# Performance work log

Hardware: AMD Instinct MI355X
Metric: run time of the kernel (lower is better)

The kernel has to match this reference:

```python
import jax, jax.numpy as jnp
import numpy as np


def setup_inputs() -> dict:
    key = jax.random.key(0)
    k1, k2, k3 = jax.random.split(key, 3)
    B, H, S, D = 2, 16, 2048, 64
    q = jax.random.normal(k1, (B, H, S, D), dtype=jnp.float32)
    k = jax.random.normal(k2, (B, H, S, D), dtype=jnp.float32)
    v = jax.random.normal(k3, (B, H, S, D), dtype=jnp.float32)
    return {"q": q, "k": k, "v": v}


def reference(q, k, v):
    # q,k,v: [B,H,S,D]; causal attention with 1/sqrt(D) scaling, fp32 softmax.
    scale = 1.0 / (q.shape[-1] ** 0.5)
    scores = jnp.einsum('bhqd,bhkd->bhqk', q * scale, k)  # [B,H,S,S]
    S = scores.shape[-1]
    causal_mask = jnp.triu(jnp.ones((S, S), dtype=bool), k=1)
    scores = jnp.where(causal_mask, -jnp.inf, scores)
    attn = jax.nn.softmax(scores.astype(jnp.float32), axis=-1).astype(q.dtype)
    output = jnp.einsum('bhqk,bhkd->bhqd', attn, v)
    # Module also returns an all-zeros attn_weights placeholder of shape [B,H,S,S]
    attn_weights = jnp.zeros(scores.shape, dtype=q.dtype)
    return (output, attn_weights)
```

## Files before the change

kernel.cpp:

```cpp
#include <hip/hip_runtime.h>


typedef __bf16 bf16x8 __attribute__((ext_vector_type(8)));
typedef float f32x4 __attribute__((ext_vector_type(4)));

#define LOG2E 1.44269504088896340736f

__device__ __forceinline__ unsigned short f2bf(float f) {
  unsigned int u = __float_as_uint(f);
  u += 0x7fffu + ((u >> 16) & 1u);
  return (unsigned short)(u >> 16);
}

__device__ __forceinline__ void block_sync_lds() {
  asm volatile("s_waitcnt lgkmcnt(0)" ::: "memory");
  __builtin_amdgcn_s_barrier();
}

__device__ __forceinline__ float redmax_q(float x) {
  float a = x, b = x;
  asm volatile("" : "+v"(b));
  asm("v_permlane16_swap_b32 %0, %1" : "+v"(a), "+v"(b));
  float m = fmaxf(a, b);
  float c = m, d = m;
  asm volatile("" : "+v"(d));
  asm("v_permlane32_swap_b32 %0, %1" : "+v"(c), "+v"(d));
  return fmaxf(c, d);
}
__device__ __forceinline__ float redsum_q(float x) {
  float a = x, b = x;
  asm volatile("" : "+v"(b));
  asm("v_permlane16_swap_b32 %0, %1" : "+v"(a), "+v"(b));
  float s = a + b;
  float c = s, d = s;
  asm volatile("" : "+v"(d));
  asm("v_permlane32_swap_b32 %0, %1" : "+v"(c), "+v"(d));
  return c + d;
}

constexpr int Sdim = 2048, Ddim = 64, BHn = 32;
constexpr int STiles = 16;
constexpr int LDA = 68;
constexpr int OUT0 = BHn * Sdim * Ddim;
constexpr int NCOMPUTE = BHn * STiles;
constexpr int NFILL = 1024;
constexpr size_t FILL_F4_PER_BLK = 32768;

__device__ __forceinline__ int vswz_m(int d) { return ((d >> 2) ^ (d >> 5)) & 7; }
__device__ __forceinline__ int vrow(int d) { return (d & 56) | ((d ^ (d >> 3)) & 7); }

__global__ __launch_bounds__(256, 3)
void flash_causal_kernel(const float* __restrict__ Q, const float* __restrict__ K,
                         const float* __restrict__ V, float* __restrict__ out) {
  __shared__ unsigned short Klds[2][64 * LDA];
  __shared__ unsigned short Vlds[2][64 * LDA];
  __shared__ unsigned short Plds[4][2][16 * LDA];

  const int tid = threadIdx.x;
  const int b   = (int)blockIdx.x;

  if (b >= NCOMPUTE) {
    const int fidx = b - NCOMPUTE;
    f32x4* zp = (f32x4*)(out + OUT0) + (size_t)fidx * FILL_F4_PER_BLK;
    const f32x4 z4 = (f32x4){0.f, 0.f, 0.f, 0.f};
    #pragma unroll 4
    for (size_t i = tid; i < FILL_F4_PER_BLK; i += 256)
      __builtin_nontemporal_store(z4, zp + i);
    return;
  }

  const int wave = tid >> 6;
  const int lane = tid & 63;
  const int quad = lane >> 4;
  const int l15  = lane & 15;

  const int bh = b & (BHn - 1);
  const int g  = b >> 5;
  const int s  = (g & 1) ? (STiles - 1) - (g >> 1) : (g >> 1);
  const int jmax = 2 * s + 1;

  const int base  = bh * Sdim * Ddim;
  const int qbase = s * 128;

  bf16x8 aq[2][2];
  #pragma unroll
  for (int f = 0; f < 2; ++f) {
    const float* qp = Q + base + (qbase + 64 * f + wave * 16 + l15) * Ddim + quad * 8;
    #pragma unroll
    for (int s2 = 0; s2 < 2; ++s2) {
      float4 a = *(const float4*)(qp + 32 * s2);
      float4 bq = *(const float4*)(qp + 32 * s2 + 4);
      union { unsigned short u[8]; bf16x8 v; } u;
      u.u[0] = f2bf(a.x * 0.125f);  u.u[1] = f2bf(a.y * 0.125f);
      u.u[2] = f2bf(a.z * 0.125f);  u.u[3] = f2bf(a.w * 0.125f);
      u.u[4] = f2bf(bq.x * 0.125f); u.u[5] = f2bf(bq.y * 0.125f);
      u.u[6] = f2bf(bq.z * 0.125f); u.u[7] = f2bf(bq.w * 0.125f);
      aq[f][s2] = u.v;
    }
  }

  f32x4 ot[2][4];
  #pragma unroll
  for (int f = 0; f < 2; ++f)
    #pragma unroll
    for (int t = 0; t < 4; ++t) ot[f][t] = (f32x4){0.f, 0.f, 0.f, 0.f};
  float mrun[2] = {-__builtin_inff(), -__builtin_inff()};
  float lrun[2] = {0.f, 0.f};

  const float4* kg4 = (const float4*)(K + base);
  const float4* vg4 = (const float4*)(V + base);
  float4 kf[4], vf[4];

  auto ldtile = [&](int j) {
    const float4* kp = kg4 + j * 1024;
    const float4* vp = vg4 + j * 1024;
    #pragma unroll
    for (int i = 0; i < 4; ++i) { kf[i] = kp[i * 256 + tid]; vf[i] = vp[i * 256 + tid]; }
  };
  auto stage = [&](int buf) {
    #pragma unroll
    for (int i = 0; i < 4; ++i) {
      int lin = i * 256 + tid;
      int row = lin >> 4;
      int c4  = (lin & 15) << 2;
      uint2 t2;
      t2.x = (unsigned int)f2bf(kf[i].x) | ((unsigned int)f2bf(kf[i].y) << 16);
      t2.y = (unsigned int)f2bf(kf[i].z) | ((unsigned int)f2bf(kf[i].w) << 16);
      *(uint2*)&Klds[buf][row * LDA + c4] = t2;
      const int sw = vswz_m(c4) << 3;
      Vlds[buf][vrow(c4 + 0) * LDA + (row ^ sw)] = f2bf(vf[i].x);
      Vlds[buf][vrow(c4 + 1) * LDA + (row ^ sw)] = f2bf(vf[i].y);
      Vlds[buf][vrow(c4 + 2) * LDA + (row ^ sw)] = f2bf(vf[i].z);
      Vlds[buf][vrow(c4 + 3) * LDA + (row ^ sw)] = f2bf(vf[i].w);
    }
  };

  ldtile(0); stage(0); ldtile(1);

  for (int j = 0; j <= jmax; ++j) {
    block_sync_lds();
    if (j < jmax) stage((j + 1) & 1);
    if (j + 2 <= jmax) ldtile(j + 2);

    const unsigned short* Kb = Klds[j & 1];
    const unsigned short* Vb = Vlds[j & 1];
    const bool f0act = (j <= 2 * s);

    f32x4 sc[2][4];
    #pragma unroll
    for (int f = 0; f < 2; ++f)
      #pragma unroll
      for (int t = 0; t < 4; ++t) sc[f][t] = (f32x4){0.f, 0.f, 0.f, 0.f};
    __builtin_amdgcn_s_setprio(1);
    #pragma unroll
    for (int s2 = 0; s2 < 2; ++s2) {
      #pragma unroll
      for (int t = 0; t < 4; ++t) {
        bf16x8 ka = *(const bf16x8*)&Kb[(16 * t + l15) * LDA + 32 * s2 + quad * 8];
        sc[0][t] = __builtin_amdgcn_mfma_f32_16x16x32_bf16(ka, aq[0][s2], sc[0][t], 0, 0, 0);
        sc[1][t] = __builtin_amdgcn_mfma_f32_16x16x32_bf16(ka, aq[1][s2], sc[1][t], 0, 0, 0);
      }
    }
    __builtin_amdgcn_s_setprio(0);

    #pragma unroll
    for (int f = 0; f < 2; ++f) {
      if (j == 2 * s + f) {
        const int qml = wave * 16 + l15;
        #pragma unroll
        for (int t = 0; t < 4; ++t)
          #pragma unroll
          for (int r = 0; r < 4; ++r)
            if (16 * t + 4 * quad + r > qml) sc[f][t][r] = -__builtin_inff();
      }
    }

    #pragma unroll
    for (int f = 0; f < 2; ++f) {
      if (f == 0 && !f0act) continue;
      float tmx[4];
      #pragma unroll
      for (int t = 0; t < 4; ++t)
        tmx[t] = fmaxf(fmaxf(sc[f][t][0], sc[f][t][1]),
                       fmaxf(sc[f][t][2], sc[f][t][3]));
      float mx = fmaxf(fmaxf(tmx[0], tmx[1]), fmaxf(tmx[2], tmx[3]));
      mx = redmax_q(mx);
      float mn    = fmaxf(mrun[f], mx);
      float alpha = __builtin_amdgcn_exp2f((mrun[f] - mn) * LOG2E);
      float msc   = mn * LOG2E;
      mrun[f] = mn;
      float rsp[4];
      #pragma unroll
      for (int t = 0; t < 4; ++t) {
        float p0 = __builtin_amdgcn_exp2f(fmaf(sc[f][t][0], LOG2E, -msc));
        float p1 = __builtin_amdgcn_exp2f(fmaf(sc[f][t][1], LOG2E, -msc));
        float p2 = __builtin_amdgcn_exp2f(fmaf(sc[f][t][2], LOG2E, -msc));
        float p3 = __builtin_amdgcn_exp2f(fmaf(sc[f][t][3], LOG2E, -msc));
        sc[f][t][0] = p0; sc[f][t][1] = p1; sc[f][t][2] = p2; sc[f][t][3] = p3;
        rsp[t] = (p0 + p1) + (p2 + p3);
      }
      float rs = (rsp[0] + rsp[1]) + (rsp[2] + rsp[3]);
      rs = redsum_q(rs);
      lrun[f] = lrun[f] * alpha + rs;
      #pragma unroll
      for (int t = 0; t < 4; ++t) {
        uint2 pw;
        pw.x = (unsigned int)f2bf(sc[f][t][0]) | ((unsigned int)f2bf(sc[f][t][1]) << 16);
        pw.y = (unsigned int)f2bf(sc[f][t][2]) | ((unsigned int)f2bf(sc[f][t][3]) << 16);
        *(uint2*)&Plds[wave][f][l15 * LDA + 16 * t + 4 * quad] = pw;
      }
      #pragma unroll
      for (int t = 0; t < 4; ++t)
        #pragma unroll
        for (int r = 0; r < 4; ++r) ot[f][t][r] *= alpha;
    }

    __builtin_amdgcn_s_setprio(1);
    #pragma unroll
    for (int s2 = 0; s2 < 2; ++s2) {
      bf16x8 pb0, pb1;
      if (f0act) pb0 = *(const bf16x8*)&Plds[wave][0][l15 * LDA + 32 * s2 + quad * 8];
      pb1 = *(const bf16x8*)&Plds[wave][1][l15 * LDA + 32 * s2 + quad * 8];
      #pragma unroll
      for (int t = 0; t < 4; ++t) {
        const int d = 16 * t + l15;
        bf16x8 va = *(const bf16x8*)&Vb[vrow(d) * LDA + (((4 * s2 + quad) ^ vswz_m(d)) << 3)];
        if (f0act)
          ot[0][t] = __builtin_amdgcn_mfma_f32_16x16x32_bf16(va, pb0, ot[0][t], 0, 0, 0);
        ot[1][t] = __builtin_amdgcn_mfma_f32_16x16x32_bf16(va, pb1, ot[1][t], 0, 0, 0);
      }
    }
    __builtin_amdgcn_s_setprio(0);
  }

  #pragma unroll
  for (int f = 0; f < 2; ++f) {
    float inv = 1.0f / lrun[f];
    float* orow = out + base + (qbase + 64 * f + wave * 16 + l15) * Ddim + 4 * quad;
    #pragma unroll
    for (int t = 0; t < 4; ++t) {
      f32x4 o4;
      o4.x = ot[f][t][0] * inv; o4.y = ot[f][t][1] * inv;
      o4.z = ot[f][t][2] * inv; o4.w = ot[f][t][3] * inv;
      *(f32x4*)(orow + 16 * t) = o4;
    }
  }
}

extern "C" void kernel_launch(void* const* d_in, const int* in_sizes, int n_in,
                              void* d_out, int out_size, void* d_ws, size_t ws_size,
                              hipStream_t stream) {
  const float* q = (const float*)d_in[0];
  const float* k = (const float*)d_in[1];
  const float* v = (const float*)d_in[2];
  float* out = (float*)d_out;
  dim3 grid(NCOMPUTE + NFILL);
  flash_causal_kernel<<<grid, dim3(256), 0, stream>>>(q, k, v, out);
}
```

Baseline: 612.4 us.

## Fold zero-fill into compute blocks via extra waves and restage after MMA

The separate zero-fill blocks are removed. Each attention block now runs two extra waves that write its share of the zero attn_weights output, stepping in lockstep with the compute waves' barriers so the fill traffic overlaps the attention work. The K/V prefetch is also restructured: the next tile is loaded at loop start and converted into LDS after the PV MMAs, with one tile in flight instead of two. The aim is to hide the bandwidth-bound fill under compute and cut the register pressure of the prefetch. In exchange, blocks grow to 384 threads, which may reduce occupancy, and the shallower prefetch exposes more load latency.

```diff
diff --git a/kernel.cpp b/kernel.cpp
--- a/kernel.cpp
+++ b/kernel.cpp
@@ -42,42 +42,52 @@
 constexpr int STiles = 16;
 constexpr int LDA = 68;
 constexpr int OUT0 = BHn * Sdim * Ddim;
-constexpr int NCOMPUTE = BHn * STiles;
-constexpr int NFILL = 1024;
-constexpr size_t FILL_F4_PER_BLK = 32768;
+constexpr int FILL_F4_PER_BLK = 65536;
+constexpr int FILL_F4_PER_SLOT = 2048;
 
 __device__ __forceinline__ int vswz_m(int d) { return ((d >> 2) ^ (d >> 5)) & 7; }
 __device__ __forceinline__ int vrow(int d) { return (d & 56) | ((d ^ (d >> 3)) & 7); }
 
-__global__ __launch_bounds__(256, 3)
+__global__ __launch_bounds__(384, 3)
 void flash_causal_kernel(const float* __restrict__ Q, const float* __restrict__ K,
                          const float* __restrict__ V, float* __restrict__ out) {
   __shared__ unsigned short Klds[2][64 * LDA];
   __shared__ unsigned short Vlds[2][64 * LDA];
   __shared__ unsigned short Plds[4][2][16 * LDA];
 
-  const int tid = threadIdx.x;
-  const int b   = (int)blockIdx.x;
-
-  if (b >= NCOMPUTE) {
-    const int fidx = b - NCOMPUTE;
-    f32x4* zp = (f32x4*)(out + OUT0) + (size_t)fidx * FILL_F4_PER_BLK;
-    const f32x4 z4 = (f32x4){0.f, 0.f, 0.f, 0.f};
-    #pragma unroll 4
-    for (size_t i = tid; i < FILL_F4_PER_BLK; i += 256)
-      __builtin_nontemporal_store(z4, zp + i);
-    return;
-  }
-
+  const int tid  = threadIdx.x;
   const int wave = tid >> 6;
   const int lane = tid & 63;
   const int quad = lane >> 4;
   const int l15  = lane & 15;
 
-  const int bh = b & (BHn - 1);
-  const int g  = b >> 5;
+  const int bh = blockIdx.x & (BHn - 1);
+  const int g  = (int)(blockIdx.x >> 5);
   const int s  = (g & 1) ? (STiles - 1) - (g >> 1) : (g >> 1);
   const int jmax = 2 * s + 1;
+
+  if (wave >= 4) {
+    f32x4* const zb = (f32x4*)(out + OUT0)
+                    + (size_t)blockIdx.x * FILL_F4_PER_BLK
+                    + (wave - 4) * 1024 + lane;
+    const f32x4 z4 = (f32x4){0.f, 0.f, 0.f, 0.f};
+    for (int j = 0; j <= jmax; ++j) {
+      block_sync_lds();
+      if (j < 32) {
+        f32x4* zp = zb + (size_t)j * FILL_F4_PER_SLOT;
+        #pragma unroll
+        for (int k = 0; k < 16; ++k)
+          __builtin_nontemporal_store(z4, zp + k * 64);
+      }
+    }
+    for (int c = jmax + 1; c < 32; ++c) {
+      f32x4* zp = zb + (size_t)c * FILL_F4_PER_SLOT;
+      #pragma unroll
+      for (int k = 0; k < 16; ++k)
+        __builtin_nontemporal_store(z4, zp + k * 64);
+    }
+    return;
+  }
 
   const int base  = bh * Sdim * Ddim;
   const int qbase = s * 128;
@@ -135,12 +145,11 @@
     }
   };
 
-  ldtile(0); stage(0); ldtile(1);
+  ldtile(0); stage(0);
 
   for (int j = 0; j <= jmax; ++j) {
     block_sync_lds();
-    if (j < jmax) stage((j + 1) & 1);
-    if (j + 2 <= jmax) ldtile(j + 2);
+    if (j < jmax) ldtile(j + 1);
 
     const unsigned short* Kb = Klds[j & 1];
     const unsigned short* Vb = Vlds[j & 1];
@@ -231,6 +240,8 @@
       }
     }
     __builtin_amdgcn_s_setprio(0);
+
+    if (j < jmax) stage((j + 1) & 1);
   }
 
   #pragma unroll
@@ -254,6 +265,6 @@
   const float* k = (const float*)d_in[1];
   const float* v = (const float*)d_in[2];
   float* out = (float*)d_out;
-  dim3 grid(NCOMPUTE + NFILL);
-  flash_causal_kernel<<<grid, dim3(256), 0, stream>>>(q, k, v, out);
-}
+  dim3 grid(BHn * STiles);
+  flash_causal_kernel<<<grid, dim3(384), 0, stream>>>(q, k, v, out);
+}
```

Result: slower. 691.0 us (+12.8%).
